# Performance work log

Measured on AMD Instinct MI355X. Metric: run time of the kernel, lower is better.

## Reference

```python
import jax, jax.numpy as jnp
import numpy as np
import math
from jax import lax

HEADS = 16
EPS = 1e-5


def dw_conv_bn(x, w, gamma, beta, mean, var):
    # x: (b, c, h, w), w: (c, 1, 5, 5) depthwise conv, then inference-mode BN
    y = lax.conv_general_dilated(
        x, w, window_strides=(1, 1), padding=[(2, 2), (2, 2)],
        dimension_numbers=('NCHW', 'OIHW', 'NCHW'),
        feature_group_count=x.shape[1])
    inv = gamma / jnp.sqrt(var + EPS)
    return y * inv[None, :, None, None] + (beta - mean * inv)[None, :, None, None]


def windowify(t):
    # 'n (i h2) (j w2) c -> n (h2 w2) (i j) c' with i=j=2 (strided 2x2 sampling)
    n, H, W, c = t.shape
    h2, w2 = H // 2, W // 2
    t = t.reshape(n, 2, h2, 2, w2, c).transpose(0, 2, 4, 1, 3, 5)
    return t.reshape(n, h2 * w2, 4, c)


def setup_inputs() -> dict:
    key = jax.random.key(0)
    ks = jax.random.split(key, 8)
    b, L, d = 8, 1024, 768
    p2 = 256  # (32/2)*(32/2)
    x = jax.random.normal(ks[0], (b, L, d), jnp.float32)
    noise = jnp.zeros((1,), jnp.float32)  # unused by forward, kept for signature fidelity
    gen_adj = jax.random.normal(ks[1], (b, HEADS, p2, p2), jnp.float32)
    conv_w = jax.random.normal(ks[2], (3, d, 1, 5, 5), jnp.float32) * 0.1  # q,k,v depthwise kernels
    bn_gamma = 1.0 + 0.1 * jax.random.normal(ks[3], (3, d), jnp.float32)
    bn_beta = 0.1 * jax.random.normal(ks[4], (3, d), jnp.float32)
    bn_mean = 0.1 * jax.random.normal(ks[5], (3, d), jnp.float32)
    bn_var = jax.random.uniform(ks[6], (3, d), jnp.float32, minval=0.5, maxval=1.5)
    return {"x": x, "noise": noise, "gen_adj": gen_adj, "conv_w": conv_w,
            "bn_gamma": bn_gamma, "bn_beta": bn_beta, "bn_mean": bn_mean,
            "bn_var": bn_var, "sparsity": 8}


def reference(x, noise, gen_adj, conv_w, bn_gamma, bn_beta, bn_mean, bn_var, sparsity):
    b, L, d = x.shape
    h = int(math.sqrt(L)); w = h
    heads = HEADS
    dh = d // heads
    scale = d ** (-0.5)  # NOTE: original scales by full dim, not head dim
    h2, w2 = h // 2, w // 2
    p2 = h2 * w2
    K = sparsity

    ximg = x.reshape(b, h, w, d).transpose(0, 3, 1, 2)  # (b, d, h, w)
    q = dw_conv_bn(ximg, conv_w[0], bn_gamma[0], bn_beta[0], bn_mean[0], bn_var[0])
    k = dw_conv_bn(ximg, conv_w[1], bn_gamma[1], bn_beta[1], bn_mean[1], bn_var[1])
    v = dw_conv_bn(ximg, conv_w[2], bn_gamma[2], bn_beta[2], bn_mean[2], bn_var[2])

    def to_heads(t):  # (b, d, h, w) -> (b, heads, L, dh)
        return t.reshape(b, heads, dh, h * w).transpose(0, 1, 3, 2)

    q, k, v = to_heads(q), to_heads(k), to_heads(v)
    kv = jnp.concatenate([k, v], axis=-1)  # (b, heads, L, 2*dh)

    # top-k routing over gen_adj (b, heads, p2, p2); weights computed but unused (mul_weight='none')
    _, r_idx = lax.top_k(gen_adj, K)
    r_idx = r_idx.reshape(b * heads, p2, K)

    q_pix = windowify(q.reshape(b * heads, h, w, dh))        # (bh, p2, 4, dh)
    kv_pix = windowify(kv.reshape(b * heads, h, w, 2 * dh))  # (bh, p2, 4, 2dh)

    # KVGather: (bh, p2, K, 4, 2dh)
    kv_sel = jax.vmap(lambda kvn, idxn: kvn[idxn])(kv_pix, r_idx)
    k_sel, v_sel = kv_sel[..., :dh], kv_sel[..., dh:]

    k_sel = k_sel.reshape(b, heads, p2, K, 4, dh).transpose(0, 2, 1, 5, 3, 4).reshape(b * p2, heads, dh, K * 4)
    v_sel = v_sel.reshape(b, heads, p2, K, 4, dh).transpose(0, 2, 1, 3, 4, 5).reshape(b * p2, heads, K * 4, dh)
    q_pix = q_pix.reshape(b, heads, p2, 4, dh).transpose(0, 2, 1, 3, 4).reshape(b * p2, heads, 4, dh)

    attn = jax.nn.softmax((q_pix * scale) @ k_sel, axis=-1)  # (b*p2, heads, 4, K*4)
    o = attn @ v_sel                                          # (b*p2, heads, 4, dh)

    # '(n h2 w2) m (i j) c -> n (j h2) (i w2) (m c)'
    o = o.reshape(b, h2, w2, heads, 2, 2, dh).transpose(0, 5, 1, 4, 2, 3, 6)
    o = o.reshape(b, h, w, heads * dh)
    return o.reshape(b, h * w, d)
```

## Files before the change

### kernel.cpp

```cpp
#include <hip/hip_runtime.h>
#include <hip/hip_bf16.h>
#include <math.h>

#define D 768
#define HEADS 16
#define DH 48
#define P2 256
#define KSEL 8

#define VSTRIDE 49
#define PSTRIDE 33

__global__ __launch_bounds__(256) void prep_kernel(
    const float* __restrict__ x,
    const float* __restrict__ w,
    const float* __restrict__ gamma,
    const float* __restrict__ beta,
    const float* __restrict__ mean,
    const float* __restrict__ var,
    const float* __restrict__ adjg,
    float* __restrict__ qw, float* __restrict__ kw, float* __restrict__ vw,
    int* __restrict__ idxout)
{
    if (blockIdx.x >= 768) {
        int wave = threadIdx.x >> 6;
        int lane = threadIdx.x & 63;
        int row  = (blockIdx.x - 768) * 4 + wave;

        const float* arow = adjg + (size_t)row * P2;
        float4 av4 = *(const float4*)(arow + lane * 4);
        float vals[4] = {av4.x, av4.y, av4.z, av4.w};

        int myidx = 0;
        #pragma unroll
        for (int it = 0; it < KSEL; it++) {
            float bv = vals[0]; int bidx = lane * 4;
            #pragma unroll
            for (int s = 1; s < 4; s++)
                if (vals[s] > bv) { bv = vals[s]; bidx = lane * 4 + s; }
            #pragma unroll
            for (int m = 32; m >= 1; m >>= 1) {
                float ov = __shfl_xor(bv, m, 64);
                int   oi = __shfl_xor(bidx, m, 64);
                if (ov > bv || (ov == bv && oi < bidx)) { bv = ov; bidx = oi; }
            }
            if (lane == it) myidx = bidx;
            #pragma unroll
            for (int s = 0; s < 4; s++)
                if (lane * 4 + s == bidx) vals[s] = -INFINITY;
        }
        if (lane < KSEL)
            idxout[row * KSEL + lane] = myidx;
        return;
    }

    int bi   = blockIdx.x;
    int b    = bi / 96;
    int rem  = bi % 96;
    int y    = rem / 3;
    int chunk = rem % 3;
    int c = chunk * 256 + threadIdx.x;

    float wq[25], wk_[25], wv[25];
    const float* wp = w + (size_t)c * 25;
    #pragma unroll
    for (int i = 0; i < 25; i++) wq[i]  = wp[i];
    #pragma unroll
    for (int i = 0; i < 25; i++) wk_[i] = wp[D * 25 + i];
    #pragma unroll
    for (int i = 0; i < 25; i++) wv[i]  = wp[2 * D * 25 + i];

    float invq = gamma[c]       * rsqrtf(var[c]       + 1e-5f);
    float invk = gamma[D + c]   * rsqrtf(var[D + c]   + 1e-5f);
    float invv = gamma[2*D + c] * rsqrtf(var[2*D + c] + 1e-5f);
    float shq = beta[c]       - mean[c]       * invq;
    float shk = beta[D + c]   - mean[D + c]   * invk;
    float shv = beta[2*D + c] - mean[2*D + c] * invv;

    const float scale = 0.03608439182435161f;
    invq *= scale; shq *= scale;

    const float* xb = x + (size_t)b * 1024 * D + c;

    float a[5][5];
    bool yok[5];
    #pragma unroll
    for (int i = 0; i < 5; i++) {
        int yy = y - 2 + i;
        yok[i] = (yy >= 0 && yy < 32);
        a[i][0] = 0.f; a[i][1] = 0.f;
        a[i][2] = yok[i] ? xb[(yy * 32 + 0) * D] : 0.f;
        a[i][3] = yok[i] ? xb[(yy * 32 + 1) * D] : 0.f;
        a[i][4] = yok[i] ? xb[(yy * 32 + 2) * D] : 0.f;
    }

    int head = c / DH, cc = c % DH;
    int i0 = y & 15, A = y >> 4;
    int n = b * HEADS + head;

    for (int xx = 0; xx < 32; xx++) {
        float sq = 0.f, sk = 0.f, sv = 0.f;
        #pragma unroll
        for (int i = 0; i < 5; i++)
        #pragma unroll
        for (int j = 0; j < 5; j++) {
            float av = a[i][j];
            sq = fmaf(av, wq[i*5+j],  sq);
            sk = fmaf(av, wk_[i*5+j], sk);
            sv = fmaf(av, wv[i*5+j],  sv);
        }
        int j0 = xx & 15, Bq = xx >> 4;
        int win = i0 * 16 + j0, slot = A * 2 + Bq;
        size_t off = (((size_t)n * P2 + win) * 4 + slot) * DH + cc;
        qw[off] = sq * invq + shq;
        kw[off] = sk * invk + shk;
        vw[off] = sv * invv + shv;
        #pragma unroll
        for (int i = 0; i < 5; i++)
        #pragma unroll
        for (int j = 0; j < 4; j++)
            a[i][j] = a[i][j+1];
        int xn = xx + 3;
        bool xok = (xn < 32);
        #pragma unroll
        for (int i = 0; i < 5; i++) {
            int yy = y - 2 + i;
            a[i][4] = (yok[i] && xok) ? xb[(yy * 32 + xn) * D] : 0.f;
        }
    }
}

__global__ __launch_bounds__(256) void attn_kernel(
    const int*   __restrict__ idxin,
    const float* __restrict__ qw,
    const float* __restrict__ kw,
    const float* __restrict__ vw,
    float* __restrict__ out)
{
    __shared__ float4 vL[4][32 * 13];
    __shared__ float4 qL[4][4 * 13];
    __shared__ float  pL[4][4 * 36];

    int wave = threadIdx.x >> 6;
    int lane = threadIdx.x & 63;
    int B    = blockIdx.x;
    int n    = (B & 7) * 16 + (B >> 9);
    int wing = (B >> 3) & 63;
    int win  = wing * 4 + wave;
    int row  = n * P2 + win;
    int b    = n >> 4, head = n & 15;

    float4* vs4 = vL[wave];
    float4* qs4 = qL[wave];
    float*  ps  = pL[wave];

    int l2 = lane & 31, half = lane >> 5;
    int kk = l2 >> 2, tt = l2 & 3;
    int mywin = idxin[row * KSEL + kk];

    const float4* qp = (const float4*)(qw + ((size_t)n * P2 + win) * 192);
    if (lane < 48) {
        int r = lane / 12, c4 = lane % 12;
        qs4[r * 13 + c4] = qp[lane];
    }

    size_t gbase = (((size_t)n * P2 + mywin) * 4 + tt) * DH + half * 24;
    const float4* srcK = (const float4*)(kw + gbase);
    const float4* srcV = (const float4*)(vw + gbase);
    float4 kregh[6];
    #pragma unroll
    for (int j = 0; j < 6; j++) kregh[j] = srcK[j];
    #pragma unroll
    for (int j = 0; j < 6; j++) vs4[l2 * 13 + half * 6 + j] = srcV[j];
    __syncthreads();

    float s4[4];
    #pragma unroll
    for (int r = 0; r < 4; r++) {
        float acc = 0.f;
        #pragma unroll
        for (int j = 0; j < 6; j++) {
            float4 q4 = qs4[r * 13 + half * 6 + j];
            acc = fmaf(q4.x, kregh[j].x, acc);
            acc = fmaf(q4.y, kregh[j].y, acc);
            acc = fmaf(q4.z, kregh[j].z, acc);
            acc = fmaf(q4.w, kregh[j].w, acc);
        }
        s4[r] = acc;
    }
    #pragma unroll
    for (int r = 0; r < 4; r++)
        s4[r] += __shfl_xor(s4[r], 32, 64);

    #pragma unroll
    for (int e = 0; e < 2; e++) {
        int r = 2 * half + e;
        float sv = s4[r];
        float m = sv;
        #pragma unroll
        for (int mm = 16; mm >= 1; mm >>= 1)
            m = fmaxf(m, __shfl_xor(m, mm, 64));
        float p = __expf(sv - m);
        float sum = p;
        #pragma unroll
        for (int mm = 16; mm >= 1; mm >>= 1)
            sum += __shfl_xor(sum, mm, 64);
        ps[r * 36 + l2] = p / sum;
    }
    __syncthreads();

    if (lane < 48) {
        int r = lane / 12, c4 = lane % 12;
        const float4* psv = (const float4*)(ps + r * 36);
        float4 acc = {0.f, 0.f, 0.f, 0.f};
        #pragma unroll
        for (int k2q = 0; k2q < 8; k2q++) {
            float4 p4 = psv[k2q];
            float4 v0 = vs4[(k2q * 4 + 0) * 13 + c4];
            float4 v1 = vs4[(k2q * 4 + 1) * 13 + c4];
            float4 v2 = vs4[(k2q * 4 + 2) * 13 + c4];
            float4 v3 = vs4[(k2q * 4 + 3) * 13 + c4];
            acc.x = fmaf(p4.x, v0.x, acc.x); acc.y = fmaf(p4.x, v0.y, acc.y);
            acc.z = fmaf(p4.x, v0.z, acc.z); acc.w = fmaf(p4.x, v0.w, acc.w);
            acc.x = fmaf(p4.y, v1.x, acc.x); acc.y = fmaf(p4.y, v1.y, acc.y);
            acc.z = fmaf(p4.y, v1.z, acc.z); acc.w = fmaf(p4.y, v1.w, acc.w);
            acc.x = fmaf(p4.z, v2.x, acc.x); acc.y = fmaf(p4.z, v2.y, acc.y);
            acc.z = fmaf(p4.z, v2.z, acc.z); acc.w = fmaf(p4.z, v2.w, acc.w);
            acc.x = fmaf(p4.w, v3.x, acc.x); acc.y = fmaf(p4.w, v3.y, acc.y);
            acc.z = fmaf(p4.w, v3.z, acc.z); acc.w = fmaf(p4.w, v3.w, acc.w);
        }
        int i0 = win >> 4, j0 = win & 15;
        int Aq = r >> 1, Bq = r & 1;
        int rowp = Bq * 16 + i0, colp = Aq * 16 + j0;
        float* op = out + ((size_t)b * 1024 + rowp * 32 + colp) * D
                        + head * DH + c4 * 4;
        *(float4*)op = acc;
    }
}

__global__ __launch_bounds__(256) void fused_attn(
    const float* __restrict__ x,
    const float* __restrict__ adjg,
    const float* __restrict__ w,
    const float* __restrict__ gamma,
    const float* __restrict__ beta,
    const float* __restrict__ mean,
    const float* __restrict__ var,
    float* __restrict__ out)
{
    __shared__ float wL[3][25][48];
    __shared__ float bnI[3][48], bnS[3][48];
    __shared__ float qL[4][192];
    __shared__ float vL[4][32 * VSTRIDE];
    __shared__ float pL[4][4 * PSTRIDE];

    int tid  = threadIdx.x;
    int wave = tid >> 6, lane = tid & 63;
    int unit = blockIdx.x * 4 + wave;
    int n    = unit >> 8;
    int win  = unit & 255;
    int b    = n >> 4, head = n & 15;

    for (int j = tid; j < 3600; j += 256) {
        int chunk = j / 1200, rem = j % 1200, t = rem / 48, cc = rem % 48;
        wL[chunk][t][cc] = w[(size_t)chunk * D * 25 + (head * DH + cc) * 25 + t];
    }
    for (int j = tid; j < 144; j += 256) {
        int chunk = j / 48, cc = j % 48;
        int g = chunk * D + head * DH + cc;
        float inv = gamma[g] * rsqrtf(var[g] + 1e-5f);
        bnI[chunk][cc] = inv;
        bnS[chunk][cc] = beta[g] - mean[g] * inv;
    }
    __syncthreads();

    float* qs = qL[wave];
    float* vs = vL[wave];
    float* ps = pL[wave];

    const float* arow = adjg + ((size_t)n * P2 + win) * P2;
    float4 av4 = *(const float4*)(arow + lane * 4);
    float vals[4] = {av4.x, av4.y, av4.z, av4.w};

    int l2 = lane & 31;
    int kk = l2 >> 2, tt = l2 & 3;
    int mywin = 0;
    #pragma unroll
    for (int it = 0; it < KSEL; it++) {
        float bv = vals[0]; int bidx = lane * 4;
        #pragma unroll
        for (int s = 1; s < 4; s++)
            if (vals[s] > bv) { bv = vals[s]; bidx = lane * 4 + s; }
        #pragma unroll
        for (int m = 32; m >= 1; m >>= 1) {
            float ov = __shfl_xor(bv, m, 64);
            int   oi = __shfl_xor(bidx, m, 64);
            if (ov > bv || (ov == bv && oi < bidx)) { bv = ov; bidx = oi; }
        }
        if (kk == it) mywin = bidx;
        #pragma unroll
        for (int s = 0; s < 4; s++)
            if (lane * 4 + s == bidx) vals[s] = -INFINITY;
    }

    const float scale = 0.03608439182435161f;
    int i0 = win >> 4, j0 = win & 15;
    const float* xbh = x + (size_t)b * 1024 * D + head * DH;

    #pragma unroll
    for (int e = 0; e < 3; e++) {
        int idx = lane + 64 * e;
        int r = idx / 48, cc = idx % 48;
        int yq  = (r >> 1) * 16 + i0;
        int xq0 = (r & 1) * 16 + j0;
        float acc = 0.f;
        for (int ty = 0; ty < 5; ty++) {
            int yy = yq + ty - 2;
            if (yy < 0 || yy > 31) continue;
            for (int tx = 0; tx < 5; tx++) {
                int xx = xq0 + tx - 2;
                if (xx < 0 || xx > 31) continue;
                acc = fmaf(xbh[(size_t)(yy * 32 + xx) * D + cc],
                           wL[0][ty * 5 + tx][cc], acc);
            }
        }
        qs[idx] = (acc * bnI[0][cc] + bnS[0][cc]) * scale;
    }

    int half  = lane >> 5;
    int chunk = 1 + half;
    float accv[48];
    {
        int yk  = (tt >> 1) * 16 + (mywin >> 4);
        int xk0 = (tt & 1) * 16 + (mywin & 15);
        #pragma unroll
        for (int cc = 0; cc < 48; cc++) accv[cc] = 0.f;
        for (int ty = 0; ty < 5; ty++) {
            int yy = yk + ty - 2;
            if (yy < 0 || yy > 31) continue;
            for (int tx = 0; tx < 5; tx++) {
                int xx = xk0 + tx - 2;
                if (xx < 0 || xx > 31) continue;
                const float* px = xbh + (size_t)(yy * 32 + xx) * D;
                const float* wt = wL[chunk][ty * 5 + tx];
                #pragma unroll
                for (int c4 = 0; c4 < 12; c4++) {
                    float4 xv = *(const float4*)(px + c4 * 4);
                    accv[c4*4+0] = fmaf(xv.x, wt[c4*4+0], accv[c4*4+0]);
                    accv[c4*4+1] = fmaf(xv.y, wt[c4*4+1], accv[c4*4+1]);
                    accv[c4*4+2] = fmaf(xv.z, wt[c4*4+2], accv[c4*4+2]);
                    accv[c4*4+3] = fmaf(xv.w, wt[c4*4+3], accv[c4*4+3]);
                }
            }
        }
        #pragma unroll
        for (int cc = 0; cc < 48; cc++) {
            float val = accv[cc] * bnI[chunk][cc] + bnS[chunk][cc];
            if (half) vs[l2 * VSTRIDE + cc] = val;
            else      accv[cc] = val;
        }
    }
    __syncthreads();

    if (!half) {
        float s4[4] = {0.f, 0.f, 0.f, 0.f};
        #pragma unroll
        for (int c = 0; c < 48; c++) {
            float kc = accv[c];
            s4[0] = fmaf(qs[c],       kc, s4[0]);
            s4[1] = fmaf(qs[48 + c],  kc, s4[1]);
            s4[2] = fmaf(qs[96 + c],  kc, s4[2]);
            s4[3] = fmaf(qs[144 + c], kc, s4[3]);
        }
        #pragma unroll
        for (int r = 0; r < 4; r++) {
            float m = s4[r];
            #pragma unroll
            for (int mm = 16; mm >= 1; mm >>= 1)
                m = fmaxf(m, __shfl_xor(m, mm, 64));
            float p = __expf(s4[r] - m);
            float sum = p;
            #pragma unroll
            for (int mm = 16; mm >= 1; mm >>= 1)
                sum += __shfl_xor(sum, mm, 64);
            ps[r * PSTRIDE + l2] = p / sum;
        }
    }
    __syncthreads();

    #pragma unroll
    for (int e = 0; e < 3; e++) {
        int idx = lane + 64 * e;
        int r = idx / 48, c = idx % 48;
        float acc = 0.f;
        #pragma unroll
        for (int k2 = 0; k2 < 32; k2++)
            acc = fmaf(ps[r * PSTRIDE + k2], vs[k2 * VSTRIDE + c], acc);
        int Aq = r >> 1, Bq = r & 1;
        int rowp = Bq * 16 + i0, colp = Aq * 16 + j0;
        out[((size_t)b * 1024 + rowp * 32 + colp) * D + head * DH + c] = acc;
    }
}

extern "C" void kernel_launch(void* const* d_in, const int* in_sizes, int n_in,
                              void* d_out, int out_size, void* d_ws, size_t ws_size,
                              hipStream_t stream)
{
    const float* x     = (const float*)d_in[0];
    const float* adjg  = (const float*)d_in[2];
    const float* w     = (const float*)d_in[3];
    const float* gamma = (const float*)d_in[4];
    const float* beta  = (const float*)d_in[5];
    const float* mean  = (const float*)d_in[6];
    const float* var   = (const float*)d_in[7];

    const size_t NQKV   = (size_t)8 * HEADS * P2 * 4 * DH;
    const size_t NROWS  = (size_t)8 * HEADS * P2;
    const size_t need3  = 3 * NQKV * sizeof(float) + NROWS * KSEL * sizeof(int);

    if (ws_size >= need3) {
        float* qw  = (float*)d_ws;
        float* kw  = qw + NQKV;
        float* vw  = kw + NQKV;
        int*   idx = (int*)(vw + NQKV);
        prep_kernel<<<8960, 256, 0, stream>>>(x, w, gamma, beta, mean, var,
                                              adjg, qw, kw, vw, idx);
        attn_kernel<<<8192, 256, 0, stream>>>(idx, qw, kw, vw, (float*)d_out);
    } else {
        fused_attn<<<8192, 256, 0, stream>>>(x, adjg, w, gamma, beta, mean, var,
                                             (float*)d_out);
    }
}
```

Before: 215.4 us.

## Split depthwise conv by q/k/v and half-row, use ballot-based top-k argmax

The conv part of the prep kernel now launches six times as many blocks. Each block handles a single one of q, k or v and half of an image row, instead of all three over a full row. This cuts the per-thread register footprint (one 25-tap weight set instead of three) and raises parallelism, at the cost of reloading the input halo more often. The top-k selection replaces the paired value/index shuffle reduction with a max-only shuffle reduction followed by a ballot and lane lookup. That halves the shuffle traffic per iteration.

```diff
diff --git a/kernel.cpp b/kernel.cpp
--- a/kernel.cpp
+++ b/kernel.cpp
@@ -10,6 +10,9 @@
 
 #define VSTRIDE 49
 #define PSTRIDE 33
+
+#define CONV_BLOCKS 4608
+#define TOPK_BLOCKS 8192
 
 __global__ __launch_bounds__(256) void prep_kernel(
     const float* __restrict__ x,
@@ -22,10 +25,10 @@
     float* __restrict__ qw, float* __restrict__ kw, float* __restrict__ vw,
     int* __restrict__ idxout)
 {
-    if (blockIdx.x >= 768) {
+    if (blockIdx.x >= CONV_BLOCKS) {
         int wave = threadIdx.x >> 6;
         int lane = threadIdx.x & 63;
-        int row  = (blockIdx.x - 768) * 4 + wave;
+        int row  = (blockIdx.x - CONV_BLOCKS) * 4 + wave;
 
         const float* arow = adjg + (size_t)row * P2;
         float4 av4 = *(const float4*)(arow + lane * 4);
@@ -34,51 +37,50 @@
         int myidx = 0;
         #pragma unroll
         for (int it = 0; it < KSEL; it++) {
-            float bv = vals[0]; int bidx = lane * 4;
+            float bv = vals[0]; int bs = 0;
+            if (vals[1] > bv) { bv = vals[1]; bs = 1; }
+            if (vals[2] > bv) { bv = vals[2]; bs = 2; }
+            if (vals[3] > bv) { bv = vals[3]; bs = 3; }
+            float gv = bv;
             #pragma unroll
-            for (int s = 1; s < 4; s++)
-                if (vals[s] > bv) { bv = vals[s]; bidx = lane * 4 + s; }
-            #pragma unroll
-            for (int m = 32; m >= 1; m >>= 1) {
-                float ov = __shfl_xor(bv, m, 64);
-                int   oi = __shfl_xor(bidx, m, 64);
-                if (ov > bv || (ov == bv && oi < bidx)) { bv = ov; bidx = oi; }
-            }
-            if (lane == it) myidx = bidx;
-            #pragma unroll
-            for (int s = 0; s < 4; s++)
-                if (lane * 4 + s == bidx) vals[s] = -INFINITY;
+            for (int m = 32; m >= 1; m >>= 1)
+                gv = fmaxf(gv, __shfl_xor(gv, m, 64));
+            unsigned long long mask = __ballot(bv == gv);
+            int wlane = (int)__builtin_ctzll(mask);
+            int wslot = __shfl(bs, wlane, 64);
+            if (lane == it) myidx = wlane * 4 + wslot;
+            if (lane == wlane) vals[wslot] = -INFINITY;
         }
         if (lane < KSEL)
             idxout[row * KSEL + lane] = myidx;
         return;
     }
 
-    int bi   = blockIdx.x;
-    int b    = bi / 96;
-    int rem  = bi % 96;
-    int y    = rem / 3;
-    int chunk = rem % 3;
-    int c = chunk * 256 + threadIdx.x;
-
-    float wq[25], wk_[25], wv[25];
-    const float* wp = w + (size_t)c * 25;
-    #pragma unroll
-    for (int i = 0; i < 25; i++) wq[i]  = wp[i];
-    #pragma unroll
-    for (int i = 0; i < 25; i++) wk_[i] = wp[D * 25 + i];
-    #pragma unroll
-    for (int i = 0; i < 25; i++) wv[i]  = wp[2 * D * 25 + i];
-
-    float invq = gamma[c]       * rsqrtf(var[c]       + 1e-5f);
-    float invk = gamma[D + c]   * rsqrtf(var[D + c]   + 1e-5f);
-    float invv = gamma[2*D + c] * rsqrtf(var[2*D + c] + 1e-5f);
-    float shq = beta[c]       - mean[c]       * invq;
-    float shk = beta[D + c]   - mean[D + c]   * invk;
-    float shv = beta[2*D + c] - mean[2*D + c] * invv;
-
-    const float scale = 0.03608439182435161f;
-    invq *= scale; shq *= scale;
+    int bi    = blockIdx.x;
+    int which = bi / 1536;
+    int rem   = bi % 1536;
+    int b     = rem / 192;
+    int rem2  = rem % 192;
+    int y     = rem2 / 6;
+    int sub   = rem2 % 6;
+    int chunk = sub >> 1;
+    int xc    = sub & 1;
+    int x0    = xc * 16;
+    int c     = chunk * 256 + threadIdx.x;
+
+    float wl[25];
+    const float* wp = w + ((size_t)which * D + c) * 25;
+    #pragma unroll
+    for (int i = 0; i < 25; i++) wl[i] = wp[i];
+
+    int g = which * D + c;
+    float inv = gamma[g] * rsqrtf(var[g] + 1e-5f);
+    float sh  = beta[g] - mean[g] * inv;
+    if (which == 0) {
+        const float scale = 0.03608439182435161f;
+        inv *= scale; sh *= scale;
+    }
+    float* dst = (which == 0) ? qw : (which == 1) ? kw : vw;
 
     const float* xb = x + (size_t)b * 1024 * D + c;
 
@@ -88,33 +90,29 @@
     for (int i = 0; i < 5; i++) {
         int yy = y - 2 + i;
         yok[i] = (yy >= 0 && yy < 32);
-        a[i][0] = 0.f; a[i][1] = 0.f;
-        a[i][2] = yok[i] ? xb[(yy * 32 + 0) * D] : 0.f;
-        a[i][3] = yok[i] ? xb[(yy * 32 + 1) * D] : 0.f;
-        a[i][4] = yok[i] ? xb[(yy * 32 + 2) * D] : 0.f;
+        #pragma unroll
+        for (int j = 0; j < 5; j++) {
+            int xxc = x0 - 2 + j;
+            a[i][j] = (yok[i] && xxc >= 0 && xxc < 32)
+                      ? xb[(yy * 32 + xxc) * D] : 0.f;
+        }
     }
 
     int head = c / DH, cc = c % DH;
     int i0 = y & 15, A = y >> 4;
     int n = b * HEADS + head;
 
-    for (int xx = 0; xx < 32; xx++) {
-        float sq = 0.f, sk = 0.f, sv = 0.f;
+    for (int xx = x0; xx < x0 + 16; xx++) {
+        float s = 0.f;
         #pragma unroll
         for (int i = 0; i < 5; i++)
         #pragma unroll
-        for (int j = 0; j < 5; j++) {
-            float av = a[i][j];
-            sq = fmaf(av, wq[i*5+j],  sq);
-            sk = fmaf(av, wk_[i*5+j], sk);
-            sv = fmaf(av, wv[i*5+j],  sv);
-        }
+        for (int j = 0; j < 5; j++)
+            s = fmaf(a[i][j], wl[i*5+j], s);
         int j0 = xx & 15, Bq = xx >> 4;
         int win = i0 * 16 + j0, slot = A * 2 + Bq;
         size_t off = (((size_t)n * P2 + win) * 4 + slot) * DH + cc;
-        qw[off] = sq * invq + shq;
-        kw[off] = sk * invk + shk;
-        vw[off] = sv * invv + shv;
+        dst[off] = s * inv + sh;
         #pragma unroll
         for (int i = 0; i < 5; i++)
         #pragma unroll
@@ -423,8 +421,8 @@
         float* kw  = qw + NQKV;
         float* vw  = kw + NQKV;
         int*   idx = (int*)(vw + NQKV);
-        prep_kernel<<<8960, 256, 0, stream>>>(x, w, gamma, beta, mean, var,
-                                              adjg, qw, kw, vw, idx);
+        prep_kernel<<<CONV_BLOCKS + TOPK_BLOCKS, 256, 0, stream>>>(
+            x, w, gamma, beta, mean, var, adjg, qw, kw, vw, idx);
         attn_kernel<<<8192, 256, 0, stream>>>(idx, qw, kw, vw, (float*)d_out);
     } else {
         fused_attn<<<8192, 256, 0, stream>>>(x, adjg, w, gamma, beta, mean, var,
```

Result: faster. 209.9 us (-2.6%).
